# Performance work log

Measured on AMD Instinct MI355X. Metric: run time of the kernel, lower is better.

## Reference

```python
import jax, jax.numpy as jnp
import numpy as np

T, B = 21, 4096
H, E, V = 1024, 50, 96
PAD = 0


def setup_inputs() -> dict:
    key = jax.random.key(0)
    ks = jax.random.split(key, 10)
    s_e = 1.0 / np.sqrt(H)  # torch LSTM init scale
    emb = jax.random.normal(ks[0], (V, E), jnp.float32)
    emb = emb.at[PAD].set(0.0)  # padding_idx row is zero
    return {
        "input_ids": jax.random.randint(ks[1], (T, B), 0, V),
        "h0": jax.random.normal(ks[2], (1, B, H), jnp.float32),
        "c0": jax.random.normal(ks[3], (1, B, H), jnp.float32),
        "emb": emb,
        "W_ih": jax.random.uniform(ks[4], (4 * H, E), jnp.float32, -s_e, s_e),
        "W_hh": jax.random.uniform(ks[5], (4 * H, H), jnp.float32, -s_e, s_e),
        "b_ih": jax.random.uniform(ks[6], (4 * H,), jnp.float32, -s_e, s_e),
        "b_hh": jax.random.uniform(ks[7], (4 * H,), jnp.float32, -s_e, s_e),
        "W_out": jax.random.uniform(ks[8], (V, H), jnp.float32, -s_e, s_e),
        "b_out": jax.random.uniform(ks[9], (V,), jnp.float32, -s_e, s_e),
    }


def reference(input_ids, h0, c0, emb, W_ih, W_hh, b_ih, b_hh, W_out, b_out):
    # char_embeds: (T, B, E)
    x = emb[input_ids]
    # Precompute input projections for all timesteps in one GEMM: (T, B, 4H)
    x_proj = jnp.einsum("tbe,ge->tbg", x, W_ih) + b_ih + b_hh

    def step(carry, xp_t):
        h, c = carry  # (B, H) each
        gates = xp_t + h @ W_hh.T  # (B, 4H), torch gate order i,f,g,o
        i, f, g, o = jnp.split(gates, 4, axis=-1)
        i = jax.nn.sigmoid(i)
        f = jax.nn.sigmoid(f)
        g = jnp.tanh(g)
        o = jax.nn.sigmoid(o)
        c = f * c + i * g
        h = o * jnp.tanh(c)
        return (h, c), h

    (h_T, c_T), h_ts = jax.lax.scan(step, (h0[0], c0[0]), x_proj)
    # char_output_projection: (T, B, V)
    scores = jnp.einsum("tbh,vh->tbv", h_ts, W_out) + b_out
    return scores, (h_T[None], c_T[None])
```

## Files before the change

kernel.cpp:

```cpp
#include <hip/hip_runtime.h>
#include <hip/hip_bf16.h>


#define T_STEPS 21
#define BSZ 4096
#define HDIM 1024
#define VOCAB 96
#define EDIM 50

typedef __attribute__((ext_vector_type(8))) short short8;
typedef __attribute__((ext_vector_type(4))) float f32x4;

#define GLL16(g, l)                                                        \
  __builtin_amdgcn_global_load_lds(                                        \
      (const __attribute__((address_space(1))) void*)(g),                  \
      (__attribute__((address_space(3))) void*)(l), 16, 0, 0)

#define ASM_BARRIER() asm volatile("s_barrier" ::: "memory")
#define ASM_VMCNT8() asm volatile("s_waitcnt vmcnt(8)" ::: "memory")
#define ASM_VMCNT0() asm volatile("s_waitcnt vmcnt(0)" ::: "memory")

__device__ __forceinline__ float sigmoidf_fast(float x) {
  return 1.0f / (1.0f + __expf(-x));
}
__device__ __forceinline__ float tanhf_fast(float x) {
  return 2.0f / (1.0f + __expf(-2.0f * x)) - 1.0f;
}

__global__ void prep_convert(const float* __restrict__ Whh_f,
                             const float* __restrict__ Wout_f,
                             const float* __restrict__ h0,
                             __hip_bfloat16* __restrict__ Whh,
                             __hip_bfloat16* __restrict__ Wout,
                             __hip_bfloat16* __restrict__ hb0) {
  int idx = blockIdx.x * 256 + threadIdx.x;
  if (idx < 4 * HDIM * HDIM) {
    Whh[idx] = __float2bfloat16(Whh_f[idx]);
    hb0[idx] = __float2bfloat16(h0[idx]);
  }
  if (idx < VOCAB * HDIM) Wout[idx] = __float2bfloat16(Wout_f[idx]);
}

__global__ void prep_ptable(const float* __restrict__ emb,
                            const float* __restrict__ Wih,
                            const float* __restrict__ bih,
                            const float* __restrict__ bhh,
                            __hip_bfloat16* __restrict__ Pb) {
  int idx = blockIdx.x * 256 + threadIdx.x;
  int v = idx >> 12, g = idx & 4095;
  int gate = g >> 10, j = g & 1023;
  const float* er = emb + v * EDIM;
  const float* wr = Wih + g * EDIM;
  float s = bih[g] + bhh[g];
#pragma unroll 10
  for (int e = 0; e < EDIM; ++e) s += er[e] * wr[e];
  Pb[(size_t)(j >> 5) * 12288 + v * 128 + gate * 32 + (j & 31)] =
      __float2bfloat16(s);
}

template <bool LAST>
__global__ __launch_bounds__(256, 2) void lstm_step_kernel(
    const int* __restrict__ ids,
    const __hip_bfloat16* __restrict__ hprev,
    const __hip_bfloat16* __restrict__ Whh,
    const __hip_bfloat16* __restrict__ Pb,
    const float* __restrict__ c_in,
    float* __restrict__ c_out,
    __hip_bfloat16* __restrict__ hnext,
    float* __restrict__ hf32)
{
  __shared__ __align__(16) char smem[65536];
  __hip_bfloat16* sPb = (__hip_bfloat16*)smem;

  const int tid = threadIdx.x;
  const int wave = tid >> 6;
  const int lane = tid & 63;
  const int bid = blockIdx.x;
  const int jt = (bid & 7) * 4 + ((bid >> 3) & 3);
  const int mt = bid >> 5;
  const int m0 = mt * 128;
  const int j0 = jt * 32;

  f32x4 acc[4][4] = {};

  const int lrow = lane >> 3;
  const int lcol = ((lane & 7) ^ lrow) * 8;

  int brow_g[4];
#pragma unroll
  for (int i = 0; i < 4; ++i) {
    int n = wave * 32 + i * 8 + lrow;
    int q = n >> 6, gate = (n >> 4) & 3, u = n & 15;
    brow_g[i] = gate * HDIM + j0 + q * 16 + u;
  }
  const __hip_bfloat16* Abase =
      hprev + (size_t)(m0 + wave * 32 + lrow) * HDIM + lcol;
  const __hip_bfloat16* Bbase = Whh + lcol;

  const int mw = (wave >> 1) * 64;
  const int gn = wave & 1;
  const int u16 = lane & 15;
  const int k16q = lane >> 4;

  const int jo = gn * 16 + u16;
  const int j = j0 + jo;
  const int rb = m0 + mw + k16q * 4;
  float cpre[4][4];
#pragma unroll
  for (int mi = 0; mi < 4; ++mi)
#pragma unroll
    for (int r = 0; r < 4; ++r)
      cpre[mi][r] = c_in[(size_t)(rb + mi * 16 + r) * HDIM + j];

  const int sSlotA = wave * 32 * 64;
  const int sSlotB = wave * 32 * 64;

  {
    __hip_bfloat16* nA = (__hip_bfloat16*)smem;
    __hip_bfloat16* nB = (__hip_bfloat16*)(smem + 16384);
#pragma unroll
    for (int i = 0; i < 4; ++i) {
      GLL16(Abase + i * 8 * HDIM, &nA[sSlotA + i * 8 * 64]);
      GLL16(Bbase + (size_t)brow_g[i] * HDIM, &nB[sSlotB + i * 8 * 64]);
    }
  }

  for (int it = 0; it < 16; ++it) {
    char* curb = smem + ((it & 1) << 15);
    char* nxtb = smem + ((~it & 1) << 15);
    const __hip_bfloat16* cA = (const __hip_bfloat16*)curb;
    const __hip_bfloat16* cB = (const __hip_bfloat16*)(curb + 16384);

    ASM_BARRIER();
    if (it < 15) {
      __hip_bfloat16* nA = (__hip_bfloat16*)nxtb;
      __hip_bfloat16* nB = (__hip_bfloat16*)(nxtb + 16384);
      const int k0 = (it + 1) * 64;
#pragma unroll
      for (int i = 0; i < 4; ++i) {
        GLL16(Abase + i * 8 * HDIM + k0, &nA[sSlotA + i * 8 * 64]);
        GLL16(Bbase + (size_t)brow_g[i] * HDIM + k0, &nB[sSlotB + i * 8 * 64]);
      }
      ASM_VMCNT8();
    } else {
      ASM_VMCNT0();
    }
    ASM_BARRIER();

#pragma unroll
    for (int kk = 0; kk < 64; kk += 32) {
      const int sl = (((kk >> 3) + k16q) ^ (u16 & 7)) * 8;
      short8 af[4], bf[4];
#pragma unroll
      for (int mi = 0; mi < 4; ++mi)
        af[mi] = *(const short8*)&cA[(mw + mi * 16 + u16) * 64 + sl];
#pragma unroll
      for (int ni = 0; ni < 4; ++ni)
        bf[ni] = *(const short8*)&cB[(gn * 64 + ni * 16 + u16) * 64 + sl];
#pragma unroll
      for (int mi = 0; mi < 4; ++mi)
#pragma unroll
        for (int ni = 0; ni < 4; ++ni)
          acc[mi][ni] = __builtin_amdgcn_mfma_f32_16x16x32_bf16(
              af[mi], bf[ni], acc[mi][ni], 0, 0, 0);
    }
  }

  {
    const __hip_bfloat16* Pbj = Pb + (size_t)jt * 12288;
#pragma unroll
    for (int i = 0; i < 6; ++i)
      GLL16(Pbj + (wave * 6 + i) * 512 + lane * 8, &sPb[(wave * 6 + i) * 512]);
  }
  __syncthreads();

#pragma unroll
  for (int mi = 0; mi < 4; ++mi) {
#pragma unroll
    for (int r = 0; r < 4; ++r) {
      int row = rb + mi * 16 + r;
      int id = ids[row];
      const __hip_bfloat16* Pr = &sPb[id * 128 + jo];
      float iv = acc[mi][0][r] + __bfloat162float(Pr[0]);
      float fv = acc[mi][1][r] + __bfloat162float(Pr[32]);
      float gv = acc[mi][2][r] + __bfloat162float(Pr[64]);
      float ov = acc[mi][3][r] + __bfloat162float(Pr[96]);
      iv = sigmoidf_fast(iv);
      fv = sigmoidf_fast(fv);
      gv = tanhf_fast(gv);
      ov = sigmoidf_fast(ov);
      size_t off = (size_t)row * HDIM + j;
      float cc = fv * cpre[mi][r] + iv * gv;
      c_out[off] = cc;
      float hh = ov * tanhf_fast(cc);
      hnext[off] = __float2bfloat16(hh);
      if (LAST) hf32[off] = hh;
    }
  }
}

__global__ __launch_bounds__(256, 2) void scores_kernel(
    const __hip_bfloat16* __restrict__ h,
    const __hip_bfloat16* __restrict__ Wout,
    const float* __restrict__ bout,
    float* __restrict__ out)
{
  __shared__ __align__(16) __hip_bfloat16 sA[128 * 128];
  __shared__ __align__(16) __hip_bfloat16 sB[96 * 128];

  const int tid = threadIdx.x;
  const int wave = tid >> 6, lane = tid & 63;
  const int u16 = lane & 15, k16q = lane >> 4;
  const long r0 = (long)blockIdx.x * 128;

  f32x4 acc[2][6] = {};

  const int srow4 = lane >> 4;
  const int sslot = lane & 15;

  for (int k0 = 0; k0 < HDIM; k0 += 128) {
#pragma unroll
    for (int i = 0; i < 8; ++i) {
      int row = wave * 32 + i * 4 + srow4;
      int gg = sslot ^ (row & 15);
      GLL16(h + (r0 + row) * HDIM + k0 + gg * 8, &sA[(wave * 32 + i * 4) * 128]);
    }
#pragma unroll
    for (int i = 0; i < 6; ++i) {
      int row = wave * 24 + i * 4 + srow4;
      int gg = sslot ^ (row & 15);
      GLL16(Wout + (size_t)row * HDIM + k0 + gg * 8,
            &sB[(wave * 24 + i * 4) * 128]);
    }
    __syncthreads();
#pragma unroll
    for (int kk = 0; kk < 128; kk += 32) {
      const int sl = (((kk >> 3) + k16q) ^ u16) * 8;
      short8 af[2], bf[6];
#pragma unroll
      for (int mi = 0; mi < 2; ++mi)
        af[mi] = *(const short8*)&sA[(wave * 32 + mi * 16 + u16) * 128 + sl];
#pragma unroll
      for (int ni = 0; ni < 6; ++ni)
        bf[ni] = *(const short8*)&sB[(ni * 16 + u16) * 128 + sl];
#pragma unroll
      for (int mi = 0; mi < 2; ++mi)
#pragma unroll
        for (int ni = 0; ni < 6; ++ni)
          acc[mi][ni] = __builtin_amdgcn_mfma_f32_16x16x32_bf16(
              af[mi], bf[ni], acc[mi][ni], 0, 0, 0);
    }
    __syncthreads();
  }

#pragma unroll
  for (int ni = 0; ni < 6; ++ni) {
    int v = ni * 16 + u16;
    float bv = bout[v];
#pragma unroll
    for (int mi = 0; mi < 2; ++mi)
#pragma unroll
      for (int r = 0; r < 4; ++r) {
        long grow = r0 + wave * 32 + mi * 16 + k16q * 4 + r;
        out[grow * VOCAB + v] = acc[mi][ni][r] + bv;
      }
  }
}

extern "C" void kernel_launch(void* const* d_in, const int* in_sizes, int n_in,
                              void* d_out, int out_size, void* d_ws, size_t ws_size,
                              hipStream_t stream) {
  const int* ids = (const int*)d_in[0];
  const float* h0 = (const float*)d_in[1];
  const float* c0 = (const float*)d_in[2];
  const float* emb = (const float*)d_in[3];
  const float* Wih = (const float*)d_in[4];
  const float* Whh_f = (const float*)d_in[5];
  const float* bih = (const float*)d_in[6];
  const float* bhh = (const float*)d_in[7];
  const float* Wout_f = (const float*)d_in[8];
  const float* bout = (const float*)d_in[9];

  float* out = (float*)d_out;
  float* scores = out;
  float* hT = out + (size_t)T_STEPS * BSZ * VOCAB;
  float* cT = hT + (size_t)BSZ * HDIM;

  const size_t BH = (size_t)BSZ * HDIM;
  char* w = (char*)d_ws;
  __hip_bfloat16* Pb = (__hip_bfloat16*)w;   w += (size_t)32 * 12288 * 2;
  __hip_bfloat16* Whh = (__hip_bfloat16*)w;  w += (size_t)4 * HDIM * HDIM * 2;
  __hip_bfloat16* Wout = (__hip_bfloat16*)w; w += (size_t)VOCAB * HDIM * 2;
  __hip_bfloat16* hts = (__hip_bfloat16*)w;
  size_t base = (size_t)32 * 12288 * 2 + (size_t)4 * HDIM * HDIM * 2 +
                (size_t)VOCAB * HDIM * 2;
  const bool full = ws_size >= base + (size_t)(T_STEPS + 1) * BH * 2;

  prep_convert<<<dim3((4 * HDIM * HDIM + 255) / 256), dim3(256), 0, stream>>>(
      Whh_f, Wout_f, h0, Whh, Wout, hts);
  prep_ptable<<<dim3((VOCAB * 4096) / 256), dim3(256), 0, stream>>>(
      emb, Wih, bih, bhh, Pb);

  for (int t = 0; t < T_STEPS; ++t) {
    __hip_bfloat16* hp = hts + (full ? (size_t)t * BH : (size_t)(t & 1) * BH);
    __hip_bfloat16* hn =
        hts + (full ? (size_t)(t + 1) * BH : (size_t)((t + 1) & 1) * BH);
    const float* cin = (t == 0) ? c0 : cT;
    if (t == T_STEPS - 1) {
      lstm_step_kernel<true><<<dim3(1024), dim3(256), 0, stream>>>(
          ids + (size_t)t * BSZ, hp, Whh, Pb, cin, cT, hn, hT);
    } else {
      lstm_step_kernel<false><<<dim3(1024), dim3(256), 0, stream>>>(
          ids + (size_t)t * BSZ, hp, Whh, Pb, cin, cT, hn, nullptr);
    }
    if (!full) {
      scores_kernel<<<dim3(BSZ / 128), dim3(256), 0, stream>>>(
          hn, Wout, bout, scores + (size_t)t * BSZ * VOCAB);
    }
  }
  if (full) {
    scores_kernel<<<dim3(T_STEPS * BSZ / 128), dim3(256), 0, stream>>>(
        hts + BH, Wout, bout, scores);
  }
}
```

Measured before the change: 1.134 ms.

## Enlarge LSTM step GEMM tiles to 256x256 with 8 waves and phased prefetch

The recurrent step kernel moves from 128x128 tiles with 4 waves to 256-row by 64-hidden-unit (256 gate-column) tiles with 8 waves. It uses 128KB of LDS with double buffering split into half-tile stages that are interleaved with four MFMA phases, and raises wave priority during MFMA. The aim is more data reuse per LDS load and better overlap of global-to-LDS loads with compute. In exchange there are 256 blocks instead of 1024, which gives lower occupancy and a single wave of blocks on the device. The precomputed input-projection table is relaid out for 64-unit hidden tiles.

```diff
diff --git a/kernel.cpp b/kernel.cpp
--- a/kernel.cpp
+++ b/kernel.cpp
@@ -17,7 +17,7 @@
       (__attribute__((address_space(3))) void*)(l), 16, 0, 0)
 
 #define ASM_BARRIER() asm volatile("s_barrier" ::: "memory")
-#define ASM_VMCNT8() asm volatile("s_waitcnt vmcnt(8)" ::: "memory")
+#define ASM_VMCNT4() asm volatile("s_waitcnt vmcnt(4)" ::: "memory")
 #define ASM_VMCNT0() asm volatile("s_waitcnt vmcnt(0)" ::: "memory")
 
 __device__ __forceinline__ float sigmoidf_fast(float x) {
@@ -54,12 +54,68 @@
   float s = bih[g] + bhh[g];
 #pragma unroll 10
   for (int e = 0; e < EDIM; ++e) s += er[e] * wr[e];
-  Pb[(size_t)(j >> 5) * 12288 + v * 128 + gate * 32 + (j & 31)] =
+  Pb[(size_t)(j >> 6) * 24576 + v * 256 + gate * 64 + (j & 63)] =
       __float2bfloat16(s);
 }
 
+
+#define STAGE_A(h, kt, b)                                                   \
+  do {                                                                      \
+    GLL16(hprev + aSrc[0] + (size_t)(h) * 131072 + (size_t)(kt) * 64,       \
+          smem + ((b) << 16) + ((h) << 14) + aDst[0]);                      \
+    GLL16(hprev + aSrc[1] + (size_t)(h) * 131072 + (size_t)(kt) * 64,       \
+          smem + ((b) << 16) + ((h) << 14) + aDst[1]);                      \
+  } while (0)
+
+#define STAGE_B(h, kt, b)                                                   \
+  do {                                                                      \
+    GLL16(Whh + bSrc[h][0] + (size_t)(kt) * 64,                             \
+          smem + ((b) << 16) + bDst[h][0]);                                 \
+    GLL16(Whh + bSrc[h][1] + (size_t)(kt) * 64,                             \
+          smem + ((b) << 16) + bDst[h][1]);                                 \
+  } while (0)
+
+#define PHASE(mh, nh, STAGE_STMT, VM_STMT)                                  \
+  {                                                                         \
+    const int sl0 = ((k16q) ^ u7) * 8;                                      \
+    const int sl1 = ((4 + k16q) ^ u7) * 8;                                  \
+    short8 af0[4], bf0[2];                                                  \
+    _Pragma("unroll") for (int mi2 = 0; mi2 < 4; ++mi2)                     \
+        af0[mi2] = *(const short8*)&cA[((mh) * 128 + wr * 64 + mi2 * 16 +   \
+                                        u16) * 64 + sl0];                   \
+    _Pragma("unroll") for (int ni2 = 0; ni2 < 2; ++ni2)                     \
+        bf0[ni2] = *(const short8*)&cB[(wc * 64 + (nh) * 32 + ni2 * 16 +    \
+                                        u16) * 64 + sl0];                   \
+    STAGE_STMT;                                                             \
+    ASM_BARRIER();                                                          \
+    __builtin_amdgcn_s_setprio(1);                                          \
+    short8 af1[4], bf1[2];                                                  \
+    _Pragma("unroll") for (int mi2 = 0; mi2 < 4; ++mi2)                     \
+        af1[mi2] = *(const short8*)&cA[((mh) * 128 + wr * 64 + mi2 * 16 +   \
+                                        u16) * 64 + sl1];                   \
+    _Pragma("unroll") for (int ni2 = 0; ni2 < 2; ++ni2)                     \
+        bf1[ni2] = *(const short8*)&cB[(wc * 64 + (nh) * 32 + ni2 * 16 +    \
+                                        u16) * 64 + sl1];                   \
+    _Pragma("unroll") for (int mi2 = 0; mi2 < 4; ++mi2)                     \
+        _Pragma("unroll") for (int ni2 = 0; ni2 < 2; ++ni2)                 \
+            acc[(mh) * 4 + mi2][(nh) * 2 + ni2] =                           \
+                __builtin_amdgcn_mfma_f32_16x16x32_bf16(                    \
+                    af0[mi2], bf0[ni2],                                     \
+                    acc[(mh) * 4 + mi2][(nh) * 2 + ni2], 0, 0, 0);          \
+    _Pragma("unroll") for (int mi2 = 0; mi2 < 4; ++mi2)                     \
+        _Pragma("unroll") for (int ni2 = 0; ni2 < 2; ++ni2)                 \
+            acc[(mh) * 4 + mi2][(nh) * 2 + ni2] =                           \
+                __builtin_amdgcn_mfma_f32_16x16x32_bf16(                    \
+                    af1[mi2], bf1[ni2],                                     \
+                    acc[(mh) * 4 + mi2][(nh) * 2 + ni2], 0, 0, 0);          \
+    __builtin_amdgcn_s_setprio(0);                                          \
+    VM_STMT;                                                                \
+    __builtin_amdgcn_sched_barrier(0);                                      \
+    ASM_BARRIER();                                                          \
+  }
+
 template <bool LAST>
-__global__ __launch_bounds__(256, 2) void lstm_step_kernel(
+__global__ __launch_bounds__(512, 2) void lstm_step_kernel(
     const int* __restrict__ ids,
     const __hip_bfloat16* __restrict__ hprev,
     const __hip_bfloat16* __restrict__ Whh,
@@ -69,130 +125,119 @@
     __hip_bfloat16* __restrict__ hnext,
     float* __restrict__ hf32)
 {
-  __shared__ __align__(16) char smem[65536];
-  __hip_bfloat16* sPb = (__hip_bfloat16*)smem;
+  __shared__ __align__(16) char smem[131072];
 
   const int tid = threadIdx.x;
-  const int wave = tid >> 6;
+  const int wid = tid >> 6;
   const int lane = tid & 63;
-  const int bid = blockIdx.x;
-  const int jt = (bid & 7) * 4 + ((bid >> 3) & 3);
-  const int mt = bid >> 5;
-  const int m0 = mt * 128;
-  const int j0 = jt * 32;
-
-  f32x4 acc[4][4] = {};
-
-  const int lrow = lane >> 3;
-  const int lcol = ((lane & 7) ^ lrow) * 8;
-
-  int brow_g[4];
-#pragma unroll
-  for (int i = 0; i < 4; ++i) {
-    int n = wave * 32 + i * 8 + lrow;
-    int q = n >> 6, gate = (n >> 4) & 3, u = n & 15;
-    brow_g[i] = gate * HDIM + j0 + q * 16 + u;
-  }
-  const __hip_bfloat16* Abase =
-      hprev + (size_t)(m0 + wave * 32 + lrow) * HDIM + lcol;
-  const __hip_bfloat16* Bbase = Whh + lcol;
-
-  const int mw = (wave >> 1) * 64;
-  const int gn = wave & 1;
+  const int wr = wid >> 2;
+  const int wc = wid & 3;
   const int u16 = lane & 15;
   const int k16q = lane >> 4;
-
-  const int jo = gn * 16 + u16;
-  const int j = j0 + jo;
-  const int rb = m0 + mw + k16q * 4;
-  float cpre[4][4];
-#pragma unroll
-  for (int mi = 0; mi < 4; ++mi)
+  const int u7 = u16 & 7;
+
+  const int bid = blockIdx.x;
+  const int mt = (bid & 7) * 2 + ((bid >> 3) & 1);
+  const int jt = bid >> 4;
+  const int m0 = mt * 256;
+
+  const int lrow = lane >> 3;
+  const int swcol = ((lane & 7) ^ lrow) * 8;
+
+  size_t aSrc[2];
+  size_t bSrc[2][2];
+  int aDst[2];
+  int bDst[2][2];
+#pragma unroll
+  for (int q = 0; q < 2; ++q) {
+    const int g = wid * 2 + q;
+    aSrc[q] = (size_t)(m0 + g * 8 + lrow) * HDIM + swcol;
+    aDst[q] = g * 1024;
+#pragma unroll
+    for (int h = 0; h < 2; ++h) {
+      const int R = (g >> 2) * 64 + h * 32 + (g & 3) * 8;
+      const int n = R + lrow;
+      const int gate = (n >> 4) & 3;
+      const int uo = (n >> 6) * 16 + (n & 15);
+      bSrc[h][q] = (size_t)(gate * HDIM + jt * 64 + uo) * HDIM + swcol;
+      bDst[h][q] = 32768 + R * 128;
+    }
+  }
+
+  STAGE_A(0, 0, 0);
+  STAGE_B(0, 0, 0);
+  STAGE_A(1, 0, 0);
+  STAGE_B(1, 0, 0);
+
+  const int jcol = jt * 64 + wc * 16 + u16;
+  float cpre[8][4];
+#pragma unroll
+  for (int mi = 0; mi < 8; ++mi)
 #pragma unroll
     for (int r = 0; r < 4; ++r)
-      cpre[mi][r] = c_in[(size_t)(rb + mi * 16 + r) * HDIM + j];
-
-  const int sSlotA = wave * 32 * 64;
-  const int sSlotB = wave * 32 * 64;
+      cpre[mi][r] = c_in[(size_t)(m0 + (mi >> 2) * 128 + wr * 64 +
+                                  (mi & 3) * 16 + k16q * 4 + r) *
+                             HDIM +
+                         jcol];
+
+  STAGE_A(0, 1, 1);
+  STAGE_B(0, 1, 1);
+
+  ASM_VMCNT4();
+  ASM_BARRIER();
+
+  f32x4 acc[8][4] = {};
+
+#pragma unroll 2
+  for (int k = 0; k < 16; ++k) {
+    const int b = k & 1;
+    const int nb = b ^ 1;
+    const __hip_bfloat16* cA = (const __hip_bfloat16*)(smem + (b << 16));
+    const __hip_bfloat16* cB =
+        (const __hip_bfloat16*)(smem + (b << 16) + 32768);
+    PHASE(0, 0, { if (k < 15) STAGE_A(1, k + 1, nb); }, {});
+    PHASE(0, 1, { if (k < 15) STAGE_B(1, k + 1, nb); }, {});
+    PHASE(1, 0, { if (k < 14) STAGE_A(0, k + 2, b); }, {});
+    PHASE(1, 1, { if (k < 14) STAGE_B(0, k + 2, b); }, {
+      if (k < 14) {
+        ASM_VMCNT4();
+      } else if (k == 14) {
+        ASM_VMCNT0();
+      }
+    });
+  }
 
   {
-    __hip_bfloat16* nA = (__hip_bfloat16*)smem;
-    __hip_bfloat16* nB = (__hip_bfloat16*)(smem + 16384);
-#pragma unroll
-    for (int i = 0; i < 4; ++i) {
-      GLL16(Abase + i * 8 * HDIM, &nA[sSlotA + i * 8 * 64]);
-      GLL16(Bbase + (size_t)brow_g[i] * HDIM, &nB[sSlotB + i * 8 * 64]);
-    }
-  }
-
-  for (int it = 0; it < 16; ++it) {
-    char* curb = smem + ((it & 1) << 15);
-    char* nxtb = smem + ((~it & 1) << 15);
-    const __hip_bfloat16* cA = (const __hip_bfloat16*)curb;
-    const __hip_bfloat16* cB = (const __hip_bfloat16*)(curb + 16384);
-
-    ASM_BARRIER();
-    if (it < 15) {
-      __hip_bfloat16* nA = (__hip_bfloat16*)nxtb;
-      __hip_bfloat16* nB = (__hip_bfloat16*)(nxtb + 16384);
-      const int k0 = (it + 1) * 64;
-#pragma unroll
-      for (int i = 0; i < 4; ++i) {
-        GLL16(Abase + i * 8 * HDIM + k0, &nA[sSlotA + i * 8 * 64]);
-        GLL16(Bbase + (size_t)brow_g[i] * HDIM + k0, &nB[sSlotB + i * 8 * 64]);
-      }
-      ASM_VMCNT8();
-    } else {
-      ASM_VMCNT0();
-    }
-    ASM_BARRIER();
-
-#pragma unroll
-    for (int kk = 0; kk < 64; kk += 32) {
-      const int sl = (((kk >> 3) + k16q) ^ (u16 & 7)) * 8;
-      short8 af[4], bf[4];
-#pragma unroll
-      for (int mi = 0; mi < 4; ++mi)
-        af[mi] = *(const short8*)&cA[(mw + mi * 16 + u16) * 64 + sl];
-#pragma unroll
-      for (int ni = 0; ni < 4; ++ni)
-        bf[ni] = *(const short8*)&cB[(gn * 64 + ni * 16 + u16) * 64 + sl];
-#pragma unroll
-      for (int mi = 0; mi < 4; ++mi)
-#pragma unroll
-        for (int ni = 0; ni < 4; ++ni)
-          acc[mi][ni] = __builtin_amdgcn_mfma_f32_16x16x32_bf16(
-              af[mi], bf[ni], acc[mi][ni], 0, 0, 0);
-    }
-  }
-
-  {
-    const __hip_bfloat16* Pbj = Pb + (size_t)jt * 12288;
+    const __hip_bfloat16* Pbj = Pb + (size_t)jt * 24576;
 #pragma unroll
     for (int i = 0; i < 6; ++i)
-      GLL16(Pbj + (wave * 6 + i) * 512 + lane * 8, &sPb[(wave * 6 + i) * 512]);
-  }
-  __syncthreads();
-
-#pragma unroll
-  for (int mi = 0; mi < 4; ++mi) {
+      GLL16(Pbj + (wid * 6 + i) * 512 + lane * 8,
+            smem + (wid * 6 + i) * 1024);
+  }
+  ASM_VMCNT0();
+  ASM_BARRIER();
+
+  const __hip_bfloat16* sPb = (const __hip_bfloat16*)smem;
+  const int rb = m0 + wr * 64 + k16q * 4;
+#pragma unroll
+  for (int mi = 0; mi < 8; ++mi) {
 #pragma unroll
     for (int r = 0; r < 4; ++r) {
-      int row = rb + mi * 16 + r;
-      int id = ids[row];
-      const __hip_bfloat16* Pr = &sPb[id * 128 + jo];
+      const int row = rb + (mi >> 2) * 128 + (mi & 3) * 16 + r;
+      const int id = ids[row];
+      const __hip_bfloat16* Pr = &sPb[id * 256 + wc * 16 + u16];
       float iv = acc[mi][0][r] + __bfloat162float(Pr[0]);
-      float fv = acc[mi][1][r] + __bfloat162float(Pr[32]);
-      float gv = acc[mi][2][r] + __bfloat162float(Pr[64]);
-      float ov = acc[mi][3][r] + __bfloat162float(Pr[96]);
+      float fv = acc[mi][1][r] + __bfloat162float(Pr[64]);
+      float gv = acc[mi][2][r] + __bfloat162float(Pr[128]);
+      float ov = acc[mi][3][r] + __bfloat162float(Pr[192]);
       iv = sigmoidf_fast(iv);
       fv = sigmoidf_fast(fv);
       gv = tanhf_fast(gv);
       ov = sigmoidf_fast(ov);
-      size_t off = (size_t)row * HDIM + j;
-      float cc = fv * cpre[mi][r] + iv * gv;
+      const size_t off = (size_t)row * HDIM + jcol;
+      const float cc = fv * cpre[mi][r] + iv * gv;
       c_out[off] = cc;
-      float hh = ov * tanhf_fast(cc);
+      const float hh = ov * tanhf_fast(cc);
       hnext[off] = __float2bfloat16(hh);
       if (LAST) hf32[off] = hh;
     }
@@ -223,7 +268,8 @@
     for (int i = 0; i < 8; ++i) {
       int row = wave * 32 + i * 4 + srow4;
       int gg = sslot ^ (row & 15);
-      GLL16(h + (r0 + row) * HDIM + k0 + gg * 8, &sA[(wave * 32 + i * 4) * 128]);
+      GLL16(h + (r0 + row) * HDIM + k0 + gg * 8,
+            &sA[(wave * 32 + i * 4) * 128]);
     }
 #pragma unroll
     for (int i = 0; i < 6; ++i) {
@@ -268,8 +314,8 @@
 }
 
 extern "C" void kernel_launch(void* const* d_in, const int* in_sizes, int n_in,
-                              void* d_out, int out_size, void* d_ws, size_t ws_size,
-                              hipStream_t stream) {
+                              void* d_out, int out_size, void* d_ws,
+                              size_t ws_size, hipStream_t stream) {
   const int* ids = (const int*)d_in[0];
   const float* h0 = (const float*)d_in[1];
   const float* c0 = (const float*)d_in[2];
@@ -288,11 +334,11 @@
 
   const size_t BH = (size_t)BSZ * HDIM;
   char* w = (char*)d_ws;
-  __hip_bfloat16* Pb = (__hip_bfloat16*)w;   w += (size_t)32 * 12288 * 2;
+  __hip_bfloat16* Pb = (__hip_bfloat16*)w;   w += (size_t)16 * 24576 * 2;
   __hip_bfloat16* Whh = (__hip_bfloat16*)w;  w += (size_t)4 * HDIM * HDIM * 2;
   __hip_bfloat16* Wout = (__hip_bfloat16*)w; w += (size_t)VOCAB * HDIM * 2;
   __hip_bfloat16* hts = (__hip_bfloat16*)w;
-  size_t base = (size_t)32 * 12288 * 2 + (size_t)4 * HDIM * HDIM * 2 +
+  size_t base = (size_t)16 * 24576 * 2 + (size_t)4 * HDIM * HDIM * 2 +
                 (size_t)VOCAB * HDIM * 2;
   const bool full = ws_size >= base + (size_t)(T_STEPS + 1) * BH * 2;
 
@@ -307,10 +353,10 @@
         hts + (full ? (size_t)(t + 1) * BH : (size_t)((t + 1) & 1) * BH);
     const float* cin = (t == 0) ? c0 : cT;
     if (t == T_STEPS - 1) {
-      lstm_step_kernel<true><<<dim3(1024), dim3(256), 0, stream>>>(
+      lstm_step_kernel<true><<<dim3(256), dim3(512), 0, stream>>>(
           ids + (size_t)t * BSZ, hp, Whh, Pb, cin, cT, hn, hT);
     } else {
-      lstm_step_kernel<false><<<dim3(1024), dim3(256), 0, stream>>>(
+      lstm_step_kernel<false><<<dim3(256), dim3(512), 0, stream>>>(
           ids + (size_t)t * BSZ, hp, Whh, Pb, cin, cT, hn, nullptr);
     }
     if (!full) {
```

Result: slower. 1.336 ms (+17.8%).

## Restructure LSTM step GEMM into 256x32 tiles with triple-buffered K pipeline

Applied to the files above, without the earlier changes.

The per-step recurrent GEMM kernel moves from 256-thread blocks with 128x32 tiles and a double-buffered 64-wide K loop to 512-thread blocks with 256x32 tiles. K is now staged 32 wide through three LDS buffers, with loads issued two tiles ahead, a vmcnt(3) wait, and s_setprio around the MFMA bursts. The gate-bias table is re-laid out so the four gate values of a column sit next to each other and are read with one 8-byte LDS load. This is meant to hide global-load latency better and reuse the W_hh tile across more batch rows, at the cost of more LDS per block (72 KB), more barriers per K step, and fewer blocks.

```diff
diff --git a/kernel.cpp b/kernel.cpp
--- a/kernel.cpp
+++ b/kernel.cpp
@@ -9,6 +9,7 @@
 #define EDIM 50
 
 typedef __attribute__((ext_vector_type(8))) short short8;
+typedef __attribute__((ext_vector_type(4))) short shortx4;
 typedef __attribute__((ext_vector_type(4))) float f32x4;
 
 #define GLL16(g, l)                                                        \
@@ -17,7 +18,7 @@
       (__attribute__((address_space(3))) void*)(l), 16, 0, 0)
 
 #define ASM_BARRIER() asm volatile("s_barrier" ::: "memory")
-#define ASM_VMCNT8() asm volatile("s_waitcnt vmcnt(8)" ::: "memory")
+#define ASM_VMCNT3() asm volatile("s_waitcnt vmcnt(3)" ::: "memory")
 #define ASM_VMCNT0() asm volatile("s_waitcnt vmcnt(0)" ::: "memory")
 
 __device__ __forceinline__ float sigmoidf_fast(float x) {
@@ -25,6 +26,9 @@
 }
 __device__ __forceinline__ float tanhf_fast(float x) {
   return 2.0f / (1.0f + __expf(-2.0f * x)) - 1.0f;
+}
+__device__ __forceinline__ float b2f(short s) {
+  return __uint_as_float(((unsigned int)(unsigned short)s) << 16);
 }
 
 __global__ void prep_convert(const float* __restrict__ Whh_f,
@@ -54,12 +58,40 @@
   float s = bih[g] + bhh[g];
 #pragma unroll 10
   for (int e = 0; e < EDIM; ++e) s += er[e] * wr[e];
-  Pb[(size_t)(j >> 5) * 12288 + v * 128 + gate * 32 + (j & 31)] =
+  Pb[(size_t)(j >> 5) * 12288 + v * 128 + (j & 31) * 4 + gate] =
       __float2bfloat16(s);
 }
 
+
+#define TILE(kk, CB, SB, DOSTAGE, VMW)                                      \
+  {                                                                         \
+    const __hip_bfloat16* bufE =                                            \
+        (const __hip_bfloat16*)(smem + (CB) * 24576);                       \
+    short8 af[4], bf[4];                                                    \
+    _Pragma("unroll") for (int mi = 0; mi < 4; ++mi)                        \
+        af[mi] = *(const short8*)&bufE[a_off[mi]];                          \
+    _Pragma("unroll") for (int g = 0; g < 4; ++g)                           \
+        bf[g] = *(const short8*)&bufE[b_off[g]];                            \
+    if (DOSTAGE) {                                                          \
+      GLL16(hprev + aSrc[0] + ((kk) + 2) * 32,                              \
+            smem + (SB) * 24576 + aDstB0);                                  \
+      GLL16(hprev + aSrc[1] + ((kk) + 2) * 32,                              \
+            smem + (SB) * 24576 + aDstB1);                                  \
+      GLL16(Whh + bSrcE + ((kk) + 2) * 32, smem + (SB) * 24576 + bDstB);    \
+    }                                                                       \
+    ASM_BARRIER();                                                          \
+    __builtin_amdgcn_s_setprio(1);                                          \
+    _Pragma("unroll") for (int mi = 0; mi < 4; ++mi)                        \
+        _Pragma("unroll") for (int g = 0; g < 4; ++g)                       \
+            acc[mi][g] = __builtin_amdgcn_mfma_f32_16x16x32_bf16(           \
+                af[mi], bf[g], acc[mi][g], 0, 0, 0);                        \
+    __builtin_amdgcn_s_setprio(0);                                          \
+    VMW;                                                                    \
+    ASM_BARRIER();                                                          \
+  }
+
 template <bool LAST>
-__global__ __launch_bounds__(256, 2) void lstm_step_kernel(
+__global__ __launch_bounds__(512, 4) void lstm_step_kernel(
     const int* __restrict__ ids,
     const __hip_bfloat16* __restrict__ hprev,
     const __hip_bfloat16* __restrict__ Whh,
@@ -69,130 +101,120 @@
     __hip_bfloat16* __restrict__ hnext,
     float* __restrict__ hf32)
 {
-  __shared__ __align__(16) char smem[65536];
-  __hip_bfloat16* sPb = (__hip_bfloat16*)smem;
+  __shared__ __align__(16) char smem[73728];
 
   const int tid = threadIdx.x;
-  const int wave = tid >> 6;
+  const int wid = tid >> 6;
   const int lane = tid & 63;
-  const int bid = blockIdx.x;
-  const int jt = (bid & 7) * 4 + ((bid >> 3) & 3);
-  const int mt = bid >> 5;
-  const int m0 = mt * 128;
-  const int j0 = jt * 32;
-
-  f32x4 acc[4][4] = {};
-
-  const int lrow = lane >> 3;
-  const int lcol = ((lane & 7) ^ lrow) * 8;
-
-  int brow_g[4];
-#pragma unroll
-  for (int i = 0; i < 4; ++i) {
-    int n = wave * 32 + i * 8 + lrow;
-    int q = n >> 6, gate = (n >> 4) & 3, u = n & 15;
-    brow_g[i] = gate * HDIM + j0 + q * 16 + u;
-  }
-  const __hip_bfloat16* Abase =
-      hprev + (size_t)(m0 + wave * 32 + lrow) * HDIM + lcol;
-  const __hip_bfloat16* Bbase = Whh + lcol;
-
-  const int mw = (wave >> 1) * 64;
-  const int gn = wave & 1;
+  const int wr = wid >> 1;
+  const int wc = wid & 1;
   const int u16 = lane & 15;
   const int k16q = lane >> 4;
 
-  const int jo = gn * 16 + u16;
-  const int j = j0 + jo;
-  const int rb = m0 + mw + k16q * 4;
+  const int bid = blockIdx.x;
+  const int mt = (bid & 7) * 2 + ((bid >> 3) & 1);
+  const int jt = bid >> 4;
+  const int m0 = mt * 256;
+
+  int a_off[4], b_off[4];
+  {
+    const int S = ((u16 & 1) << 2) | k16q;
+#pragma unroll
+    for (int mi = 0; mi < 4; ++mi) {
+      const int La = wr * 32 + mi * 8 + (u16 >> 1);
+      a_off[mi] = La * 64 + (S ^ (La & 7)) * 8;
+    }
+#pragma unroll
+    for (int g = 0; g < 4; ++g) {
+      const int Lb = wc * 32 + g * 8 + (u16 >> 1);
+      b_off[g] = 8192 + Lb * 64 + (S ^ (Lb & 7)) * 8;
+    }
+  }
+
+  size_t aSrc[2];
+  size_t bSrcE;
+  const int aDstB0 = wid * 2048;
+  const int aDstB1 = wid * 2048 + 1024;
+  const int bDstB = 16384 + wid * 1024;
+  {
+    const int Sp = lane & 7;
+#pragma unroll
+    for (int i = 0; i < 2; ++i) {
+      const int La = wid * 16 + i * 8 + (lane >> 3);
+      const int S = Sp ^ (La & 7);
+      const int mrow = 2 * La + (S >> 2);
+      aSrc[i] = (size_t)(m0 + mrow) * HDIM + (S & 3) * 8;
+    }
+    const int Lb = wid * 8 + (lane >> 3);
+    const int S = Sp ^ (Lb & 7);
+    const int n = 2 * Lb + (S >> 2);
+    const int wcg = n >> 6, gate = (n >> 4) & 3, u = n & 15;
+    bSrcE = (size_t)(gate * HDIM + jt * 32 + wcg * 16 + u) * HDIM +
+            (S & 3) * 8;
+  }
+
+  GLL16(hprev + aSrc[0], smem + aDstB0);
+  GLL16(hprev + aSrc[1], smem + aDstB1);
+  GLL16(Whh + bSrcE, smem + bDstB);
+  GLL16(hprev + aSrc[0] + 32, smem + 24576 + aDstB0);
+  GLL16(hprev + aSrc[1] + 32, smem + 24576 + aDstB1);
+  GLL16(Whh + bSrcE + 32, smem + 24576 + bDstB);
+  ASM_VMCNT3();
+  ASM_BARRIER();
+
+  f32x4 acc[4][4] = {};
+
+#pragma unroll 1
+  for (int kb = 0; kb < 30; kb += 3) {
+    TILE(kb, 0, 2, true, ASM_VMCNT3());
+    TILE(kb + 1, 1, 0, true, ASM_VMCNT3());
+    TILE(kb + 2, 2, 1, true, ASM_VMCNT3());
+  }
+  TILE(30, 0, 2, false, ASM_VMCNT0());
+  TILE(31, 1, 0, false, {});
+
+  const int jcol = jt * 32 + wc * 16 + u16;
   float cpre[4][4];
 #pragma unroll
   for (int mi = 0; mi < 4; ++mi)
 #pragma unroll
     for (int r = 0; r < 4; ++r)
-      cpre[mi][r] = c_in[(size_t)(rb + mi * 16 + r) * HDIM + j];
-
-  const int sSlotA = wave * 32 * 64;
-  const int sSlotB = wave * 32 * 64;
-
-  {
-    __hip_bfloat16* nA = (__hip_bfloat16*)smem;
-    __hip_bfloat16* nB = (__hip_bfloat16*)(smem + 16384);
-#pragma unroll
-    for (int i = 0; i < 4; ++i) {
-      GLL16(Abase + i * 8 * HDIM, &nA[sSlotA + i * 8 * 64]);
-      GLL16(Bbase + (size_t)brow_g[i] * HDIM, &nB[sSlotB + i * 8 * 64]);
-    }
-  }
-
-  for (int it = 0; it < 16; ++it) {
-    char* curb = smem + ((it & 1) << 15);
-    char* nxtb = smem + ((~it & 1) << 15);
-    const __hip_bfloat16* cA = (const __hip_bfloat16*)curb;
-    const __hip_bfloat16* cB = (const __hip_bfloat16*)(curb + 16384);
-
-    ASM_BARRIER();
-    if (it < 15) {
-      __hip_bfloat16* nA = (__hip_bfloat16*)nxtb;
-      __hip_bfloat16* nB = (__hip_bfloat16*)(nxtb + 16384);
-      const int k0 = (it + 1) * 64;
-#pragma unroll
-      for (int i = 0; i < 4; ++i) {
-        GLL16(Abase + i * 8 * HDIM + k0, &nA[sSlotA + i * 8 * 64]);
-        GLL16(Bbase + (size_t)brow_g[i] * HDIM + k0, &nB[sSlotB + i * 8 * 64]);
-      }
-      ASM_VMCNT8();
-    } else {
-      ASM_VMCNT0();
-    }
-    ASM_BARRIER();
-
-#pragma unroll
-    for (int kk = 0; kk < 64; kk += 32) {
-      const int sl = (((kk >> 3) + k16q) ^ (u16 & 7)) * 8;
-      short8 af[4], bf[4];
-#pragma unroll
-      for (int mi = 0; mi < 4; ++mi)
-        af[mi] = *(const short8*)&cA[(mw + mi * 16 + u16) * 64 + sl];
-#pragma unroll
-      for (int ni = 0; ni < 4; ++ni)
-        bf[ni] = *(const short8*)&cB[(gn * 64 + ni * 16 + u16) * 64 + sl];
-#pragma unroll
-      for (int mi = 0; mi < 4; ++mi)
-#pragma unroll
-        for (int ni = 0; ni < 4; ++ni)
-          acc[mi][ni] = __builtin_amdgcn_mfma_f32_16x16x32_bf16(
-              af[mi], bf[ni], acc[mi][ni], 0, 0, 0);
-    }
-  }
+      cpre[mi][r] = c_in[(size_t)(m0 + wr * 64 + mi * 16 + k16q * 4 + r) *
+                             HDIM +
+                         jcol];
 
   {
     const __hip_bfloat16* Pbj = Pb + (size_t)jt * 12288;
 #pragma unroll
-    for (int i = 0; i < 6; ++i)
-      GLL16(Pbj + (wave * 6 + i) * 512 + lane * 8, &sPb[(wave * 6 + i) * 512]);
-  }
-  __syncthreads();
-
+    for (int i = 0; i < 3; ++i)
+      GLL16(Pbj + (wid * 3 + i) * 512 + lane * 8,
+            smem + (wid * 3 + i) * 1024);
+  }
+  ASM_VMCNT0();
+  ASM_BARRIER();
+
+  const __hip_bfloat16* sPb = (const __hip_bfloat16*)smem;
+  const int uo4 = (wc * 16 + u16) * 4;
+  const int rb = m0 + wr * 64 + k16q * 4;
 #pragma unroll
   for (int mi = 0; mi < 4; ++mi) {
 #pragma unroll
     for (int r = 0; r < 4; ++r) {
-      int row = rb + mi * 16 + r;
-      int id = ids[row];
-      const __hip_bfloat16* Pr = &sPb[id * 128 + jo];
-      float iv = acc[mi][0][r] + __bfloat162float(Pr[0]);
-      float fv = acc[mi][1][r] + __bfloat162float(Pr[32]);
-      float gv = acc[mi][2][r] + __bfloat162float(Pr[64]);
-      float ov = acc[mi][3][r] + __bfloat162float(Pr[96]);
+      const int row = rb + mi * 16 + r;
+      const int id = ids[row];
+      const shortx4 pv = *(const shortx4*)&sPb[id * 128 + uo4];
+      float iv = acc[mi][0][r] + b2f(pv[0]);
+      float fv = acc[mi][1][r] + b2f(pv[1]);
+      float gv = acc[mi][2][r] + b2f(pv[2]);
+      float ov = acc[mi][3][r] + b2f(pv[3]);
       iv = sigmoidf_fast(iv);
       fv = sigmoidf_fast(fv);
       gv = tanhf_fast(gv);
       ov = sigmoidf_fast(ov);
-      size_t off = (size_t)row * HDIM + j;
-      float cc = fv * cpre[mi][r] + iv * gv;
+      const size_t off = (size_t)row * HDIM + jcol;
+      const float cc = fv * cpre[mi][r] + iv * gv;
       c_out[off] = cc;
-      float hh = ov * tanhf_fast(cc);
+      const float hh = ov * tanhf_fast(cc);
       hnext[off] = __float2bfloat16(hh);
       if (LAST) hf32[off] = hh;
     }
@@ -223,7 +245,8 @@
     for (int i = 0; i < 8; ++i) {
       int row = wave * 32 + i * 4 + srow4;
       int gg = sslot ^ (row & 15);
-      GLL16(h + (r0 + row) * HDIM + k0 + gg * 8, &sA[(wave * 32 + i * 4) * 128]);
+      GLL16(h + (r0 + row) * HDIM + k0 + gg * 8,
+            &sA[(wave * 32 + i * 4) * 128]);
     }
 #pragma unroll
     for (int i = 0; i < 6; ++i) {
@@ -268,8 +291,8 @@
 }
 
 extern "C" void kernel_launch(void* const* d_in, const int* in_sizes, int n_in,
-                              void* d_out, int out_size, void* d_ws, size_t ws_size,
-                              hipStream_t stream) {
+                              void* d_out, int out_size, void* d_ws,
+                              size_t ws_size, hipStream_t stream) {
   const int* ids = (const int*)d_in[0];
   const float* h0 = (const float*)d_in[1];
   const float* c0 = (const float*)d_in[2];
@@ -307,10 +330,10 @@
         hts + (full ? (size_t)(t + 1) * BH : (size_t)((t + 1) & 1) * BH);
     const float* cin = (t == 0) ? c0 : cT;
     if (t == T_STEPS - 1) {
-      lstm_step_kernel<true><<<dim3(1024), dim3(256), 0, stream>>>(
+      lstm_step_kernel<true><<<dim3(512), dim3(512), 0, stream>>>(
           ids + (size_t)t * BSZ, hp, Whh, Pb, cin, cT, hn, hT);
     } else {
-      lstm_step_kernel<false><<<dim3(1024), dim3(256), 0, stream>>>(
+      lstm_step_kernel<false><<<dim3(512), dim3(512), 0, stream>>>(
           ids + (size_t)t * BSZ, hp, Whh, Pb, cin, cT, hn, nullptr);
     }
     if (!full) {
```

Result: slower. 1.170 ms (+3.2%).
